# Kernel tuning notes

Measured on AMD Instinct MI355X. Metric: run time of the kernel, lower is better.

The kernel has to match this reference:

```python
import jax, jax.numpy as jnp
import numpy as np

B, T, C, H = 2, 2048, 1024, 16
HD = C // H  # head_dim = 64

def setup_inputs() -> dict:
    key = jax.random.key(0)
    ks = jax.random.split(key, 9)
    s = 1.0 / np.sqrt(C)
    return {
        "x": jax.random.normal(ks[0], (B, T, C), dtype=jnp.float32),
        "Wk": jax.random.uniform(ks[1], (C, C), jnp.float32, -s, s),
        "bk": jax.random.uniform(ks[2], (C,), jnp.float32, -s, s),
        "Wq": jax.random.uniform(ks[3], (C, C), jnp.float32, -s, s),
        "bq": jax.random.uniform(ks[4], (C,), jnp.float32, -s, s),
        "Wv": jax.random.uniform(ks[5], (C, C), jnp.float32, -s, s),
        "bv": jax.random.uniform(ks[6], (C,), jnp.float32, -s, s),
        "Wp": jax.random.uniform(ks[7], (C, C), jnp.float32, -s, s),
        "bp": jax.random.uniform(ks[8], (C,), jnp.float32, -s, s),
    }

def reference(x, Wk, bk, Wq, bq, Wv, bv, Wp, bp):
    # Linear projections: [B,T,C] -> [B,H,T,HD]
    def split_heads(t):
        return t.reshape(B, T, H, HD).transpose(0, 2, 1, 3)
    k = split_heads(x @ Wk.T + bk)
    q = split_heads(x @ Wq.T + bq)
    v = split_heads(x @ Wv.T + bv)
    # scaled dot-product with causal mask
    att = jnp.einsum('bhtd,bhsd->bhts', q, k) * (1.0 / np.sqrt(HD))
    causal = jnp.tril(jnp.ones((T, T), dtype=bool))
    att = jnp.where(causal[None, None], att, -jnp.inf)
    att = jax.nn.softmax(att, axis=-1)
    y = jnp.einsum('bhts,bhsd->bhtd', att, v)  # [B,H,T,HD]
    y = y.transpose(0, 2, 1, 3).reshape(B, T, C)
    return y @ Wp.T + bp
```

## Files before the change

kernel.cpp:

```cpp
#include <hip/hip_runtime.h>
#include <stdint.h>

#define Bv  2
#define Tv  2048
#define Cv  1024
#define Hv  16
#define HDv 64
#define LOG2E 1.44269504088896340736f

typedef __bf16 bf16x8 __attribute__((ext_vector_type(8)));
typedef float f32x4 __attribute__((ext_vector_type(4)));
typedef unsigned short us4v __attribute__((ext_vector_type(4)));
typedef unsigned short us8v __attribute__((ext_vector_type(8)));

#define VMCNT(n) asm volatile("s_waitcnt vmcnt(" #n ")" ::: "memory")
#define LGKM0()  asm volatile("s_waitcnt lgkmcnt(0)" ::: "memory")
#define SBAR()   __builtin_amdgcn_s_barrier()
#define SCHED0() __builtin_amdgcn_sched_barrier(0)

static __device__ __forceinline__ unsigned short f2bf(float f) {
    unsigned int u = __builtin_bit_cast(unsigned int, f);
    u += 0x7FFFu + ((u >> 16) & 1u);
    return (unsigned short)(u >> 16);
}

static __device__ __forceinline__ unsigned int cvt_pk_bf16(float lo, float hi) {
    unsigned int w;
    asm("v_cvt_pk_bf16_f32 %0, %1, %2" : "=v"(w) : "v"(lo), "v"(hi));
    return w;
}

static __device__ __forceinline__ void gld_lds16(const void* g, void* l) {
    __builtin_amdgcn_global_load_lds(
        (const __attribute__((address_space(1))) void*)g,
        (__attribute__((address_space(3))) void*)l, 16, 0, 0);
}

static __device__ __forceinline__ f32x4 mfma_bf16(bf16x8 a, bf16x8 b, f32x4 c) {
    return __builtin_amdgcn_mfma_f32_16x16x32_bf16(a, b, c, 0, 0, 0);
}

__global__ __launch_bounds__(256) void cvt_all(const float* __restrict__ x,
                                               const float* __restrict__ wq,
                                               const float* __restrict__ wk,
                                               const float* __restrict__ wv,
                                               const float* __restrict__ wp,
                                               unsigned short* __restrict__ ox,
                                               unsigned short* __restrict__ oqk,
                                               unsigned short* __restrict__ ov,
                                               unsigned short* __restrict__ op) {
    const int id = blockIdx.x;
    const float* in;
    unsigned short* out;
    int blk;
    if (id < 4096)      { in = x;  out = ox;            blk = id; }
    else if (id < 5120) { in = wq; out = oqk;           blk = id - 4096; }
    else if (id < 6144) { in = wk; out = oqk + 1048576; blk = id - 5120; }
    else if (id < 7168) { in = wv; out = ov;            blk = id - 6144; }
    else                { in = wp; out = op;            blk = id - 7168; }
    int i = (blk * 256 + threadIdx.x) * 4;
    float4 v = *(const float4*)(in + i);
    us4v o;
    o[0] = f2bf(v.x); o[1] = f2bf(v.y); o[2] = f2bf(v.z); o[3] = f2bf(v.w);
    *(us4v*)(out + i) = o;
}

__global__ __launch_bounds__(256) void gemm_qkv(const unsigned short* __restrict__ X,
                                                const unsigned short* __restrict__ Wqk,
                                                const unsigned short* __restrict__ Wv,
                                                const float* __restrict__ bq,
                                                const float* __restrict__ bk,
                                                const float* __restrict__ bv,
                                                unsigned short* __restrict__ qout,
                                                unsigned short* __restrict__ vtout,
                                                float scale) {
    __shared__ unsigned short As[2][128 * 32];
    __shared__ unsigned short Bs[2][128 * 32];
    const int K = Cv;

    const int tid  = threadIdx.x;
    const int lane = tid & 63;
    const int w    = tid >> 6;
    const int wr   = w >> 1, wc = w & 1;
    const int l16  = lane & 15;
    const int lk8  = (lane >> 4) * 8;
    const int id   = blockIdx.x;

    const unsigned short *Ap, *Bp;
    int m0, n0;
    if (id < 512) {
        const int xcd = id & 7, r = id >> 3;
        const int nt  = r >> 2;
        const int mt  = (r & 3) + xcd * 4;
        Ap = X;  Bp = Wqk; m0 = mt * 128; n0 = nt * 128;
    } else {
        const int id2 = id - 512;
        const int xcd = id2 & 7, r = id2 >> 3;
        const int mt  = r >> 2;
        const int nt  = (r & 3) + xcd * 4;
        Ap = Wv; Bp = X;   m0 = mt * 128; n0 = nt * 128;
    }

    f32x4 acc[4][4] = {};
    const int srow = tid >> 2;
    const int skc  = (tid & 3) * 8;

    auto stageAB = [&](int buf, int k0) {
        gld_lds16(Ap + (size_t)(m0 + srow)      * K + k0 + skc, &As[buf][(size_t)tid * 8]);
        gld_lds16(Ap + (size_t)(m0 + srow + 64) * K + k0 + skc, &As[buf][(size_t)(tid + 256) * 8]);
        gld_lds16(Bp + (size_t)(n0 + srow)      * K + k0 + skc, &Bs[buf][(size_t)tid * 8]);
        gld_lds16(Bp + (size_t)(n0 + srow + 64) * K + k0 + skc, &Bs[buf][(size_t)(tid + 256) * 8]);
    };

    int buf = 0;
    stageAB(0, 0);
    for (int k0 = 0; k0 < K; k0 += 32) {
        if (k0 + 32 < K) { stageAB(buf ^ 1, k0 + 32); VMCNT(4); }
        else             VMCNT(0);
        SBAR(); SCHED0();

        bf16x8 af[4], bf[4];
#pragma unroll
        for (int mf = 0; mf < 4; ++mf)
            af[mf] = *(const bf16x8*)&As[buf][(wr * 64 + mf * 16 + l16) * 32 + lk8];
#pragma unroll
        for (int nf = 0; nf < 4; ++nf)
            bf[nf] = *(const bf16x8*)&Bs[buf][(wc * 64 + nf * 16 + l16) * 32 + lk8];
#pragma unroll
        for (int mf = 0; mf < 4; ++mf)
#pragma unroll
            for (int nf = 0; nf < 4; ++nf)
                acc[mf][nf] = mfma_bf16(af[mf], bf[nf], acc[mf][nf]);

        LGKM0(); SBAR();
        buf ^= 1;
    }

    if (id < 512) {
#pragma unroll
        for (int mf = 0; mf < 4; ++mf)
#pragma unroll
            for (int nf = 0; nf < 4; ++nf)
#pragma unroll
                for (int r = 0; r < 4; ++r) {
                    int m = m0 + wr * 64 + mf * 16 + (lane >> 4) * 4 + r;
                    int n = n0 + wc * 64 + nf * 16 + l16;
                    int sel = n >> 10, ch = n & 1023;
                    float bia = sel ? bk[ch] : bq[ch];
                    float v = (acc[mf][nf][r] + bia) * (sel ? 1.0f : scale);
                    int b = m >> 11, t = m & (Tv - 1);
                    int h = ch >> 6, d = ch & (HDv - 1);
                    qout[(size_t)sel * 4194304 +
                         (((size_t)(b * Hv + h)) * Tv + t) * HDv + d] = f2bf(v);
                }
    } else {
#pragma unroll
        for (int mf = 0; mf < 4; ++mf)
#pragma unroll
            for (int nf = 0; nf < 4; ++nf)
#pragma unroll
                for (int r = 0; r < 4; ++r) {
                    int m = m0 + wr * 64 + mf * 16 + (lane >> 4) * 4 + r;
                    int n = n0 + wc * 64 + nf * 16 + l16;
                    float v = acc[mf][nf][r] + bv[m];
                    vtout[((size_t)(n >> 11) * 1024 + m) * Tv + (n & (Tv - 1))] = f2bf(v);
                }
    }
}

__global__ __launch_bounds__(256) void gemm_64(const unsigned short* __restrict__ A,
                                               const unsigned short* __restrict__ Bm,
                                               const float* __restrict__ bias0,
                                               float* __restrict__ out,
                                               int N, int K) {
    __shared__ unsigned short As[2][128 * 64];
    __shared__ unsigned short Bs[2][64 * 64];

    const int tid  = threadIdx.x;
    const int lane = tid & 63;
    const int w    = tid >> 6;
    const int wr   = w >> 1, wc = w & 1;
    const int m0   = blockIdx.y * 128;
    const int n0   = blockIdx.x * 64;
    const int l16  = lane & 15;
    const int lk   = (lane >> 4);

    f32x4 acc[4][2] = {};

    auto stageAB = [&](int buf, int k0) {
#pragma unroll
        for (int i = 0; i < 4; ++i) {
            int ch = i * 256 + tid, r = ch >> 3, cs = ch & 7, c = cs ^ (r & 7);
            gld_lds16(A + (size_t)(m0 + r) * K + k0 + c * 8, &As[buf][(size_t)ch * 8]);
        }
#pragma unroll
        for (int i = 0; i < 2; ++i) {
            int ch = i * 256 + tid, r = ch >> 3, cs = ch & 7, c = cs ^ (r & 7);
            gld_lds16(Bm + (size_t)(n0 + r) * K + k0 + c * 8, &Bs[buf][(size_t)ch * 8]);
        }
    };

    int buf = 0;
    stageAB(0, 0);
    for (int k0 = 0; k0 < K; k0 += 64) {
        if (k0 + 64 < K) { stageAB(buf ^ 1, k0 + 64); VMCNT(6); }
        else             VMCNT(0);
        SBAR(); SCHED0();

#pragma unroll
        for (int ks = 0; ks < 2; ++ks) {
            bf16x8 af[4], bf[2];
#pragma unroll
            for (int mf = 0; mf < 4; ++mf) {
                int row = wr * 64 + mf * 16 + l16;
                af[mf] = *(const bf16x8*)&As[buf][(row * 8 + ((ks * 4 + lk) ^ (row & 7))) * 8];
            }
#pragma unroll
            for (int nf = 0; nf < 2; ++nf) {
                int row = wc * 32 + nf * 16 + l16;
                bf[nf] = *(const bf16x8*)&Bs[buf][(row * 8 + ((ks * 4 + lk) ^ (row & 7))) * 8];
            }
#pragma unroll
            for (int mf = 0; mf < 4; ++mf)
#pragma unroll
                for (int nf = 0; nf < 2; ++nf)
                    acc[mf][nf] = mfma_bf16(af[mf], bf[nf], acc[mf][nf]);
        }

        LGKM0(); SBAR();
        buf ^= 1;
    }

#pragma unroll
    for (int mf = 0; mf < 4; ++mf)
#pragma unroll
        for (int nf = 0; nf < 2; ++nf)
#pragma unroll
            for (int r = 0; r < 4; ++r) {
                int m = m0 + wr * 64 + mf * 16 + (lane >> 4) * 4 + r;
                int n = n0 + wc * 32 + nf * 16 + l16;
                out[(size_t)m * N + n] = acc[mf][nf][r] + bias0[n];
            }
}

__global__ __launch_bounds__(256) void attn_kernel(const unsigned short* __restrict__ q,
                                                   const unsigned short* __restrict__ k,
                                                   const unsigned short* __restrict__ vt,
                                                   unsigned short* __restrict__ y) {
    __shared__ __align__(16) unsigned short Ks[2][64 * 64];
    __shared__ __align__(16) unsigned short Vs[2][64 * 64];
    __shared__ __align__(16) unsigned short Pb[4][16 * 64];

    const int tid  = threadIdx.x;
    const int lane = tid & 63;
    const int w    = tid >> 6;
    const int l16  = lane & 15;
    const int lk   = lane >> 4;

    const int lb   = blockIdx.x;
    const int xcd  = lb & 7;
    const int rest = lb >> 3;
    const int bh   = xcd * 4 + (rest >> 4);
    const int p    = rest & 15;

    const int b = bh >> 4, h = bh & (Hv - 1);
    const size_t head_off = (size_t)bh * (Tv * HDv);
    const unsigned short* kpb = k  + head_off;
    const unsigned short* vpb = vt + head_off;
    unsigned short* pb = &Pb[w][0];
    const int key3 = l16 & 7;
    const int kg0  = (lk ^ key3) * 8;
    const int kg1  = ((4 + lk) ^ key3) * 8;

    bf16x8 ones;
    {
        us8v o;
#pragma unroll
        for (int i = 0; i < 8; ++i) o[i] = 0x3F80;
        ones = __builtin_bit_cast(bf16x8, o);
    }

    auto stage = [&](int buf, int kk0) {
#pragma unroll
        for (int i = 0; i < 2; ++i) {
            int ch = i * 256 + tid;
            int r  = ch >> 3, cs = ch & 7, c = cs ^ (r & 7);
            gld_lds16(kpb + (size_t)(kk0 + r) * HDv + c * 8, &Ks[buf][ch * 8]);
        }
#pragma unroll
        for (int i = 0; i < 2; ++i) {
            int ch = i * 256 + tid;
            int r  = ch >> 3, cs = ch & 7, c = cs ^ (r & 7);
            gld_lds16(vpb + (size_t)r * Tv + kk0 + c * 8, &Vs[buf][ch * 8]);
        }
    };

    for (int ph = 0; ph < 2; ++ph) {
        const int tile = ph ? (31 - p) : p;
        const int qr0  = tile * 64 + w * 16;
        const int qg   = qr0 + l16;
        const int nkt  = tile + 1;

        bf16x8 qf0, qf1;
        {
            const unsigned short* qp = q + head_off + (size_t)qg * HDv + lk * 8;
            qf0 = *(const bf16x8*)qp;
            qf1 = *(const bf16x8*)(qp + 32);
        }

        f32x4 acc[4] = {};
        f32x4 lacc = {};

        int cur = 0;
        stage(0, 0);

        for (int j = 0; j < nkt; ++j) {
            const int kk0 = j * 64;
            VMCNT(0); SBAR(); SCHED0();
            if (j + 1 < nkt) stage(cur ^ 1, kk0 + 64);

            f32x4 s[4];
            __builtin_amdgcn_s_setprio(1);
#pragma unroll
            for (int ct = 0; ct < 4; ++ct) {
                const int rb = (ct * 16 + l16) * 64;
                bf16x8 k0 = *(const bf16x8*)&Ks[cur][rb + kg0];
                bf16x8 k1 = *(const bf16x8*)&Ks[cur][rb + kg1];
                f32x4 z = {};
                z = mfma_bf16(k0, qf0, z);
                z = mfma_bf16(k1, qf1, z);
                s[ct] = z;
            }
            __builtin_amdgcn_s_setprio(0);

            if (kk0 + 63 > qr0) {
#pragma unroll
                for (int ct = 0; ct < 4; ++ct) {
                    const int kb2 = kk0 + ct * 16 + lk * 4;
#pragma unroll
                    for (int r = 0; r < 4; ++r)
                        if (kb2 + r > qg) s[ct][r] = -1e38f;
                }
            }

#pragma unroll
            for (int ct = 0; ct < 4; ++ct)
#pragma unroll
                for (int r = 0; r < 4; ++r)
                    s[ct][r] = __builtin_exp2f(s[ct][r] - 16.0f);

#pragma unroll
            for (int ct = 0; ct < 4; ++ct) {
                uint2 wv;
                wv.x = cvt_pk_bf16(s[ct][0], s[ct][1]);
                wv.y = cvt_pk_bf16(s[ct][2], s[ct][3]);
                int gp = (((ct * 2 + (lk >> 1)) ^ key3) * 8) + (lk & 1) * 4;
                *(uint2*)&pb[l16 * 64 + gp] = wv;
            }

            __builtin_amdgcn_s_setprio(1);
#pragma unroll
            for (int kh = 0; kh < 2; ++kh) {
                const int vg = ((kh * 4 + lk) ^ key3) * 8;
                bf16x8 pf = *(const bf16x8*)&pb[l16 * 64 + vg];
#pragma unroll
                for (int nt = 0; nt < 4; ++nt) {
                    bf16x8 vfr = *(const bf16x8*)&Vs[cur][(nt * 16 + l16) * 64 + vg];
                    acc[nt] = mfma_bf16(vfr, pf, acc[nt]);
                }
                lacc = mfma_bf16(ones, pf, lacc);
            }
            __builtin_amdgcn_s_setprio(0);

            cur ^= 1;
        }

        const float rl = 1.0f / lacc[0];
        const size_t ybase = ((size_t)(b * Tv + qg)) * Cv + h * HDv + lk * 4;
#pragma unroll
        for (int nt = 0; nt < 4; ++nt) {
            uint2 wv;
            wv.x = cvt_pk_bf16(acc[nt][0] * rl, acc[nt][1] * rl);
            wv.y = cvt_pk_bf16(acc[nt][2] * rl, acc[nt][3] * rl);
            *(uint2*)&y[ybase + nt * 16] = wv;
        }

        SBAR();
    }
}

extern "C" void kernel_launch(void* const* d_in, const int* in_sizes, int n_in,
                              void* d_out, int out_size, void* d_ws, size_t ws_size,
                              hipStream_t stream) {
    const float* x  = (const float*)d_in[0];
    const float* Wk = (const float*)d_in[1];
    const float* bk = (const float*)d_in[2];
    const float* Wq = (const float*)d_in[3];
    const float* bq = (const float*)d_in[4];
    const float* Wv = (const float*)d_in[5];
    const float* bv = (const float*)d_in[6];
    const float* Wp = (const float*)d_in[7];
    const float* bp = (const float*)d_in[8];

    unsigned short* ws   = (unsigned short*)d_ws;
    unsigned short* xb   = ws;
    unsigned short* wqkb = xb   + 4194304;
    unsigned short* wvb  = wqkb + 2097152;
    unsigned short* wpb  = wvb  + 1048576;
    unsigned short* qb   = wpb  + 1048576;
    unsigned short* kb   = qb   + 4194304;
    unsigned short* vtb  = kb   + 4194304;
    unsigned short* yb   = xb;
    (void)kb;

    cvt_all<<<8192, 256, 0, stream>>>(x, Wq, Wk, Wv, Wp, xb, wqkb, wvb, wpb);

    gemm_qkv<<<768, 256, 0, stream>>>(xb, wqkb, wvb, bq, bk, bv, qb, vtb,
                                      0.125f * LOG2E);

    attn_kernel<<<512, 256, 0, stream>>>(qb, kb, vtb, yb);

    dim3 gp(Cv / 64, (Bv * Tv) / 128);
    gemm_64<<<gp, 256, 0, stream>>>(yb, wpb, bp, (float*)d_out, Cv, Cv);
}
```

Before: 127.0 us.

## Split attention KV loop across two wave groups and widen QKV GEMM K-tile

The attention kernel now launches 512 threads per block. Two groups of four waves each process alternating 64-key tiles for the same query rows, and their partial outputs and row sums are combined through shared memory before the final write. The QKV GEMM moves to a 64-wide K tile with XOR-swizzled LDS staging. Both GEMMs switch to a single barrier per iteration that waits for the load, then issues the next prefetch, so the trailing LGKM wait and barrier are gone. The aim is more waves per CU for the latency-bound attention loop and fewer barriers in the GEMMs. The cost is more LDS per block, an extra cross-group reduction step, and prefetches that overlap less with compute.

```diff
diff --git a/kernel.cpp b/kernel.cpp
--- a/kernel.cpp
+++ b/kernel.cpp
@@ -74,8 +74,8 @@
                                                 unsigned short* __restrict__ qout,
                                                 unsigned short* __restrict__ vtout,
                                                 float scale) {
-    __shared__ unsigned short As[2][128 * 32];
-    __shared__ unsigned short Bs[2][128 * 32];
+    __shared__ __align__(16) unsigned short As[2][128 * 64];
+    __shared__ __align__(16) unsigned short Bs[2][128 * 64];
     const int K = Cv;
 
     const int tid  = threadIdx.x;
@@ -83,7 +83,7 @@
     const int w    = tid >> 6;
     const int wr   = w >> 1, wc = w & 1;
     const int l16  = lane & 15;
-    const int lk8  = (lane >> 4) * 8;
+    const int lk   = lane >> 4;
     const int id   = blockIdx.x;
 
     const unsigned short *Ap, *Bp;
@@ -102,37 +102,45 @@
     }
 
     f32x4 acc[4][4] = {};
-    const int srow = tid >> 2;
-    const int skc  = (tid & 3) * 8;
 
     auto stageAB = [&](int buf, int k0) {
-        gld_lds16(Ap + (size_t)(m0 + srow)      * K + k0 + skc, &As[buf][(size_t)tid * 8]);
-        gld_lds16(Ap + (size_t)(m0 + srow + 64) * K + k0 + skc, &As[buf][(size_t)(tid + 256) * 8]);
-        gld_lds16(Bp + (size_t)(n0 + srow)      * K + k0 + skc, &Bs[buf][(size_t)tid * 8]);
-        gld_lds16(Bp + (size_t)(n0 + srow + 64) * K + k0 + skc, &Bs[buf][(size_t)(tid + 256) * 8]);
+#pragma unroll
+        for (int i = 0; i < 4; ++i) {
+            int ch = i * 256 + tid, r = ch >> 3, cs = ch & 7, c = cs ^ (r & 7);
+            gld_lds16(Ap + (size_t)(m0 + r) * K + k0 + c * 8, &As[buf][(size_t)ch * 8]);
+        }
+#pragma unroll
+        for (int i = 0; i < 4; ++i) {
+            int ch = i * 256 + tid, r = ch >> 3, cs = ch & 7, c = cs ^ (r & 7);
+            gld_lds16(Bp + (size_t)(n0 + r) * K + k0 + c * 8, &Bs[buf][(size_t)ch * 8]);
+        }
     };
 
     int buf = 0;
     stageAB(0, 0);
-    for (int k0 = 0; k0 < K; k0 += 32) {
-        if (k0 + 32 < K) { stageAB(buf ^ 1, k0 + 32); VMCNT(4); }
-        else             VMCNT(0);
-        SBAR(); SCHED0();
-
-        bf16x8 af[4], bf[4];
-#pragma unroll
-        for (int mf = 0; mf < 4; ++mf)
-            af[mf] = *(const bf16x8*)&As[buf][(wr * 64 + mf * 16 + l16) * 32 + lk8];
-#pragma unroll
-        for (int nf = 0; nf < 4; ++nf)
-            bf[nf] = *(const bf16x8*)&Bs[buf][(wc * 64 + nf * 16 + l16) * 32 + lk8];
-#pragma unroll
-        for (int mf = 0; mf < 4; ++mf)
-#pragma unroll
-            for (int nf = 0; nf < 4; ++nf)
-                acc[mf][nf] = mfma_bf16(af[mf], bf[nf], acc[mf][nf]);
-
-        LGKM0(); SBAR();
+    for (int k0 = 0; k0 < K; k0 += 64) {
+        VMCNT(0); SBAR(); SCHED0();
+        if (k0 + 64 < K) stageAB(buf ^ 1, k0 + 64);
+
+#pragma unroll
+        for (int ks = 0; ks < 2; ++ks) {
+            bf16x8 af[4], bf[4];
+#pragma unroll
+            for (int mf = 0; mf < 4; ++mf) {
+                int row = wr * 64 + mf * 16 + l16;
+                af[mf] = *(const bf16x8*)&As[buf][(row * 8 + ((ks * 4 + lk) ^ (row & 7))) * 8];
+            }
+#pragma unroll
+            for (int nf = 0; nf < 4; ++nf) {
+                int row = wc * 64 + nf * 16 + l16;
+                bf[nf] = *(const bf16x8*)&Bs[buf][(row * 8 + ((ks * 4 + lk) ^ (row & 7))) * 8];
+            }
+#pragma unroll
+            for (int mf = 0; mf < 4; ++mf)
+#pragma unroll
+                for (int nf = 0; nf < 4; ++nf)
+                    acc[mf][nf] = mfma_bf16(af[mf], bf[nf], acc[mf][nf]);
+        }
         buf ^= 1;
     }
 
@@ -203,9 +211,8 @@
     int buf = 0;
     stageAB(0, 0);
     for (int k0 = 0; k0 < K; k0 += 64) {
-        if (k0 + 64 < K) { stageAB(buf ^ 1, k0 + 64); VMCNT(6); }
-        else             VMCNT(0);
-        SBAR(); SCHED0();
+        VMCNT(0); SBAR(); SCHED0();
+        if (k0 + 64 < K) stageAB(buf ^ 1, k0 + 64);
 
 #pragma unroll
         for (int ks = 0; ks < 2; ++ks) {
@@ -226,8 +233,6 @@
                 for (int nf = 0; nf < 2; ++nf)
                     acc[mf][nf] = mfma_bf16(af[mf], bf[nf], acc[mf][nf]);
         }
-
-        LGKM0(); SBAR();
         buf ^= 1;
     }
 
@@ -243,17 +248,20 @@
             }
 }
 
-__global__ __launch_bounds__(256) void attn_kernel(const unsigned short* __restrict__ q,
+__global__ __launch_bounds__(512) void attn_kernel(const unsigned short* __restrict__ q,
                                                    const unsigned short* __restrict__ k,
                                                    const unsigned short* __restrict__ vt,
                                                    unsigned short* __restrict__ y) {
-    __shared__ __align__(16) unsigned short Ks[2][64 * 64];
-    __shared__ __align__(16) unsigned short Vs[2][64 * 64];
-    __shared__ __align__(16) unsigned short Pb[4][16 * 64];
+    __shared__ __align__(16) unsigned short Ks[2][2][64 * 64];
+    __shared__ __align__(16) unsigned short Vs[2][2][64 * 64];
+    __shared__ __align__(16) unsigned short Pb[8][16 * 64];
 
     const int tid  = threadIdx.x;
     const int lane = tid & 63;
     const int w    = tid >> 6;
+    const int grp  = w >> 2;
+    const int wl   = w & 3;
+    const int gtid = tid & 255;
     const int l16  = lane & 15;
     const int lk   = lane >> 4;
 
@@ -283,23 +291,24 @@
     auto stage = [&](int buf, int kk0) {
 #pragma unroll
         for (int i = 0; i < 2; ++i) {
-            int ch = i * 256 + tid;
+            int ch = i * 256 + gtid;
             int r  = ch >> 3, cs = ch & 7, c = cs ^ (r & 7);
-            gld_lds16(kpb + (size_t)(kk0 + r) * HDv + c * 8, &Ks[buf][ch * 8]);
+            gld_lds16(kpb + (size_t)(kk0 + r) * HDv + c * 8, &Ks[grp][buf][ch * 8]);
         }
 #pragma unroll
         for (int i = 0; i < 2; ++i) {
-            int ch = i * 256 + tid;
+            int ch = i * 256 + gtid;
             int r  = ch >> 3, cs = ch & 7, c = cs ^ (r & 7);
-            gld_lds16(vpb + (size_t)r * Tv + kk0 + c * 8, &Vs[buf][ch * 8]);
+            gld_lds16(vpb + (size_t)r * Tv + kk0 + c * 8, &Vs[grp][buf][ch * 8]);
         }
     };
 
     for (int ph = 0; ph < 2; ++ph) {
         const int tile = ph ? (31 - p) : p;
-        const int qr0  = tile * 64 + w * 16;
+        const int qr0  = tile * 64 + wl * 16;
         const int qg   = qr0 + l16;
         const int nkt  = tile + 1;
+        const int NIT  = (nkt + 1) >> 1;
 
         bf16x8 qf0, qf1;
         {
@@ -310,81 +319,95 @@
 
         f32x4 acc[4] = {};
         f32x4 lacc = {};
-
         int cur = 0;
-        stage(0, 0);
-
-        for (int j = 0; j < nkt; ++j) {
+        if (grp < nkt) stage(0, grp * 64);
+
+        for (int i = 0; i < NIT; ++i) {
+            const int j   = 2 * i + grp;
             const int kk0 = j * 64;
             VMCNT(0); SBAR(); SCHED0();
-            if (j + 1 < nkt) stage(cur ^ 1, kk0 + 64);
-
-            f32x4 s[4];
-            __builtin_amdgcn_s_setprio(1);
-#pragma unroll
-            for (int ct = 0; ct < 4; ++ct) {
-                const int rb = (ct * 16 + l16) * 64;
-                bf16x8 k0 = *(const bf16x8*)&Ks[cur][rb + kg0];
-                bf16x8 k1 = *(const bf16x8*)&Ks[cur][rb + kg1];
-                f32x4 z = {};
-                z = mfma_bf16(k0, qf0, z);
-                z = mfma_bf16(k1, qf1, z);
-                s[ct] = z;
-            }
-            __builtin_amdgcn_s_setprio(0);
-
-            if (kk0 + 63 > qr0) {
+            if (j + 2 < nkt) stage(cur ^ 1, kk0 + 128);
+
+            if (j < nkt) {
+                f32x4 s[4];
+                __builtin_amdgcn_s_setprio(1);
 #pragma unroll
                 for (int ct = 0; ct < 4; ++ct) {
-                    const int kb2 = kk0 + ct * 16 + lk * 4;
+                    const int rb = (ct * 16 + l16) * 64;
+                    bf16x8 k0 = *(const bf16x8*)&Ks[grp][cur][rb + kg0];
+                    bf16x8 k1 = *(const bf16x8*)&Ks[grp][cur][rb + kg1];
+                    f32x4 z = {};
+                    z = mfma_bf16(k0, qf0, z);
+                    z = mfma_bf16(k1, qf1, z);
+                    s[ct] = z;
+                }
+                __builtin_amdgcn_s_setprio(0);
+
+                if (kk0 + 63 > qr0) {
+#pragma unroll
+                    for (int ct = 0; ct < 4; ++ct) {
+                        const int kb2 = kk0 + ct * 16 + lk * 4;
+#pragma unroll
+                        for (int r = 0; r < 4; ++r)
+                            if (kb2 + r > qg) s[ct][r] = -1e38f;
+                    }
+                }
+
+#pragma unroll
+                for (int ct = 0; ct < 4; ++ct)
 #pragma unroll
                     for (int r = 0; r < 4; ++r)
-                        if (kb2 + r > qg) s[ct][r] = -1e38f;
-                }
-            }
-
-#pragma unroll
-            for (int ct = 0; ct < 4; ++ct)
-#pragma unroll
-                for (int r = 0; r < 4; ++r)
-                    s[ct][r] = __builtin_exp2f(s[ct][r] - 16.0f);
-
-#pragma unroll
-            for (int ct = 0; ct < 4; ++ct) {
+                        s[ct][r] = __builtin_exp2f(s[ct][r] - 16.0f);
+
+#pragma unroll
+                for (int ct = 0; ct < 4; ++ct) {
+                    uint2 wv;
+                    wv.x = cvt_pk_bf16(s[ct][0], s[ct][1]);
+                    wv.y = cvt_pk_bf16(s[ct][2], s[ct][3]);
+                    int gp = (((ct * 2 + (lk >> 1)) ^ key3) * 8) + (lk & 1) * 4;
+                    *(uint2*)&pb[l16 * 64 + gp] = wv;
+                }
+
+                __builtin_amdgcn_s_setprio(1);
+#pragma unroll
+                for (int kh = 0; kh < 2; ++kh) {
+                    const int vg = ((kh * 4 + lk) ^ key3) * 8;
+                    bf16x8 pf = *(const bf16x8*)&pb[l16 * 64 + vg];
+#pragma unroll
+                    for (int nt = 0; nt < 4; ++nt) {
+                        bf16x8 vfr = *(const bf16x8*)&Vs[grp][cur][(nt * 16 + l16) * 64 + vg];
+                        acc[nt] = mfma_bf16(vfr, pf, acc[nt]);
+                    }
+                    lacc = mfma_bf16(ones, pf, lacc);
+                }
+                __builtin_amdgcn_s_setprio(0);
+            }
+            cur ^= 1;
+        }
+
+        f32x4* cb = (f32x4*)&Ks[1][0][0];
+        float*  lf = (float*)&Pb[0][0];
+        const int base = wl * 64 + lane;
+        SBAR();
+        if (grp == 1) {
+#pragma unroll
+            for (int nt = 0; nt < 4; ++nt) cb[nt * 256 + base] = acc[nt];
+            lf[base] = lacc[0];
+        }
+        LGKM0(); SBAR();
+        if (grp == 0) {
+#pragma unroll
+            for (int nt = 0; nt < 4; ++nt) acc[nt] += cb[nt * 256 + base];
+            const float rl = 1.0f / (lacc[0] + lf[base]);
+            const size_t ybase = ((size_t)(b * Tv + qg)) * Cv + h * HDv + lk * 4;
+#pragma unroll
+            for (int nt = 0; nt < 4; ++nt) {
                 uint2 wv;
-                wv.x = cvt_pk_bf16(s[ct][0], s[ct][1]);
-                wv.y = cvt_pk_bf16(s[ct][2], s[ct][3]);
-                int gp = (((ct * 2 + (lk >> 1)) ^ key3) * 8) + (lk & 1) * 4;
-                *(uint2*)&pb[l16 * 64 + gp] = wv;
-            }
-
-            __builtin_amdgcn_s_setprio(1);
-#pragma unroll
-            for (int kh = 0; kh < 2; ++kh) {
-                const int vg = ((kh * 4 + lk) ^ key3) * 8;
-                bf16x8 pf = *(const bf16x8*)&pb[l16 * 64 + vg];
-#pragma unroll
-                for (int nt = 0; nt < 4; ++nt) {
-                    bf16x8 vfr = *(const bf16x8*)&Vs[cur][(nt * 16 + l16) * 64 + vg];
-                    acc[nt] = mfma_bf16(vfr, pf, acc[nt]);
-                }
-                lacc = mfma_bf16(ones, pf, lacc);
-            }
-            __builtin_amdgcn_s_setprio(0);
-
-            cur ^= 1;
-        }
-
-        const float rl = 1.0f / lacc[0];
-        const size_t ybase = ((size_t)(b * Tv + qg)) * Cv + h * HDv + lk * 4;
-#pragma unroll
-        for (int nt = 0; nt < 4; ++nt) {
-            uint2 wv;
-            wv.x = cvt_pk_bf16(acc[nt][0] * rl, acc[nt][1] * rl);
-            wv.y = cvt_pk_bf16(acc[nt][2] * rl, acc[nt][3] * rl);
-            *(uint2*)&y[ybase + nt * 16] = wv;
-        }
-
+                wv.x = cvt_pk_bf16(acc[nt][0] * rl, acc[nt][1] * rl);
+                wv.y = cvt_pk_bf16(acc[nt][2] * rl, acc[nt][3] * rl);
+                *(uint2*)&y[ybase + nt * 16] = wv;
+            }
+        }
         SBAR();
     }
 }
@@ -418,7 +441,7 @@
     gemm_qkv<<<768, 256, 0, stream>>>(xb, wqkb, wvb, bq, bk, bv, qb, vtb,
                                       0.125f * LOG2E);
 
-    attn_kernel<<<512, 256, 0, stream>>>(qb, kb, vtb, yb);
+    attn_kernel<<<512, 512, 0, stream>>>(qb, kb, vtb, yb);
 
     dim3 gp(Cv / 64, (Bv * Tv) / 128);
     gemm_64<<<gp, 256, 0, stream>>>(yb, wpb, bp, (float*)d_out, Cv, Cv);
```

After: 105.4 us. -17.0%, faster.
